# Optimization experiments

Measured on AMD Instinct MI355X. Metric: run time of the kernel, lower is better.

The kernel has to match this reference:

```python
import jax, jax.numpy as jnp
import numpy as np

B, L_Q, S_KV, H, E = 4, 1024, 1024, 8, 64
IN_CH = OUT_CH = 512
MODES = 64
INDEX_Q = np.arange(MODES)   # 'lowest' mode selection -> range(0, modes)
INDEX_KV = np.arange(MODES)
SCALE = 1.0 / np.sqrt(OUT_CH)
FACTOR = 5


def setup_inputs() -> dict:
    key = jax.random.key(0)
    ks = jax.random.split(key, 7)
    tf_queries = jax.random.normal(ks[0], (B, L_Q, H, E), jnp.float32)
    queries = jax.random.normal(ks[1], (B, L_Q, H, E), jnp.float32)
    keys = jax.random.normal(ks[2], (B, S_KV, H, E), jnp.float32)
    values = jax.random.normal(ks[3], (B, S_KV, H, E), jnp.float32)
    mask = jnp.ones((1,), jnp.int32)  # unused by the module
    weights_fuse = jax.random.uniform(ks[4], (H, L_Q, 2), jnp.float32)
    # torch.rand with cfloat dtype samples re/im independently from U[0,1)
    w1_re = SCALE * jax.random.uniform(ks[5], (H, IN_CH // 8, OUT_CH // 8, MODES), jnp.float32)
    w1_im = SCALE * jax.random.uniform(ks[6], (H, IN_CH // 8, OUT_CH // 8, MODES), jnp.float32)
    return dict(tf_queries=tf_queries, queries=queries, keys=keys, values=values,
                mask=mask, weights_fuse=weights_fuse, w1_re=w1_re, w1_im=w1_im)


def get_sig_scores(n, queries, keys, scale, corr):
    # queries/keys: [B, L, H, E] (keys already aligned to L_Q)
    B_, Lq, H_, E_ = queries.shape
    Lk = keys.shape[1]
    q = jnp.transpose(queries, (0, 2, 1, 3))  # [B,H,L,E]
    k = jnp.transpose(keys, (0, 2, 1, 3))
    if corr:
        qf = jnp.fft.rfft(jnp.transpose(queries, (0, 2, 3, 1)), axis=-1)
        kf = jnp.fft.rfft(jnp.transpose(keys, (0, 2, 3, 1)), axis=-1)
        autocorr = jnp.transpose(jnp.fft.irfft(qf * jnp.conj(kf), axis=-1), (0, 1, 3, 2))  # [B,H,L,E]
    else:
        autocorr = q
    amp = jnp.linalg.norm(autocorr, axis=-1)           # [B,H,L]
    _, top_idx = jax.lax.top_k(amp, n)                 # [B,H,n]
    q_sel = jnp.take_along_axis(q, top_idx[..., None], axis=2)  # [B,H,n,E]
    scores = jnp.einsum('bhnd,bhmd->bhnm', q_sel, k) * scale    # [B,H,n,Lk]
    full = jnp.full((B_, H_, Lq, Lk), -jnp.inf, scores.dtype)
    bi = jnp.arange(B_)[:, None, None]
    hi = jnp.arange(H_)[None, :, None]
    full = full.at[bi, hi, top_idx].set(scores)        # scatter selected query rows
    # softmax over the query axis for every key position (transpose(2,3))
    return jax.nn.softmax(jnp.swapaxes(full, 2, 3), axis=-1)  # [B,H,Lk,Lq]


def reference(tf_queries, queries, keys, values, mask, weights_fuse, w1_re, w1_im):
    B_, Lq, H_, E_ = queries.shape
    S_ = keys.shape[1]
    xq = jnp.transpose(queries, (0, 2, 3, 1))  # [B,H,E,L_Q]
    xk = jnp.transpose(keys, (0, 2, 3, 1))     # [B,H,E,S]
    if Lq > S_:
        pad = jnp.zeros((B_, Lq - S_, H_, E_), keys.dtype)
        keys2 = jnp.concatenate([keys, pad], axis=1)
        values2 = jnp.concatenate([values, pad], axis=1)
    else:
        keys2 = keys[:, :Lq]
        values2 = values[:, :Lq]
    n_top = min(int(FACTOR * np.ceil(np.log(Lq))), Lq)

    attn_t = get_sig_scores(n_top, queries, keys2, SCALE, corr=True)
    attn_tf = get_sig_scores(n_top, tf_queries, keys2, SCALE, corr=False)

    nw = jax.nn.softmax(weights_fuse, axis=-1)  # [H,L_Q,2]
    fused = nw[None, :, :, 0, None] * attn_t + nw[None, :, :, 1, None] * attn_tf
    # dropout(p=0.1) in eval mode -> identity

    xq_ft = jnp.fft.rfft(xq, axis=-1)[:, :, :, INDEX_Q]   # [B,H,E,M]
    xk_ft = jnp.fft.rfft(xk, axis=-1)[:, :, :, INDEX_KV]  # [B,H,E,M]
    xqk = jnp.tanh(jnp.einsum('bhex,bhey->bhxy', xq_ft, xk_ft))  # complex tanh
    xqkv = jnp.einsum('bhxy,bhey->bhex', xqk, xk_ft)
    w1 = w1_re + 1j * w1_im
    xqkvw = jnp.einsum('bhex,heox->bhox', xqkv, w1)        # [B,H,O,M]
    out_ft = jnp.zeros((B_, H_, E_, Lq // 2 + 1), xqkvw.dtype)
    out_ft = out_ft.at[:, :, :, INDEX_Q].set(xqkvw)
    out = jnp.fft.irfft(out_ft / IN_CH / OUT_CH, n=Lq, axis=-1)  # [B,H,E,L_Q]

    output = jnp.einsum('bhlm,bhmd->bhld', fused, jnp.transpose(values2, (0, 2, 1, 3)))
    output = jnp.transpose(output, (0, 1, 3, 2))  # [B,H,D,L_Q]
    return (output + out) * 0.5
```

## Files before the change

kernel.cpp:

```cpp
#include <hip/hip_runtime.h>
#include <math.h>

#define B_ 4
#define H_ 8
#define L_ 1024
#define E_ 64
#define NTOP 35
#define SCALE_ 0.04419417382415922f

__global__ __launch_bounds__(256) void k_stage(const float* __restrict__ q_g,
                                               const float* __restrict__ k_g,
                                               float* __restrict__ xtq,
                                               float* __restrict__ xtk) {
  __shared__ float tile[64][65];
  const int tc = blockIdx.x & 15;
  const int src = (blockIdx.x >> 4) & 1;
  const int bh = blockIdx.x >> 5;
  const int b = bh >> 3, h = bh & 7;
  const int t0 = tc * 64;
  const int tid = threadIdx.x;
  const float* in = src ? k_g : q_g;
  float* out = src ? xtk : xtq;

  for (int idx = tid; idx < 1024; idx += 256) {
    int t = idx >> 4, e4 = idx & 15;
    float4 v = reinterpret_cast<const float4*>(
        in + ((size_t)(b * L_ + t0 + t) * H_ + h) * E_)[e4];
    tile[t][e4 * 4 + 0] = v.x; tile[t][e4 * 4 + 1] = v.y;
    tile[t][e4 * 4 + 2] = v.z; tile[t][e4 * 4 + 3] = v.w;
  }
  __syncthreads();
  for (int idx = tid; idx < 1024; idx += 256) {
    int e = idx >> 4, t4 = idx & 15;
    float4 v = make_float4(tile[t4 * 4 + 0][e], tile[t4 * 4 + 1][e],
                           tile[t4 * 4 + 2][e], tile[t4 * 4 + 3][e]);
    reinterpret_cast<float4*>(out + ((size_t)(bh * 64 + e)) * 1024 + t0)[t4] = v;
  }
}

__global__ __launch_bounds__(512) void k_fft_c(const float* __restrict__ xtq,
                                               const float* __restrict__ xtk,
                                               float* __restrict__ amp2_part,
                                               float* __restrict__ qft,
                                               float* __restrict__ kft) {
  __shared__ __align__(16) float zre[4][1024], zim[4][1024];
  __shared__ float ctab[512], stab[512];
  const int eg = blockIdx.x & 15;
  const int bh = blockIdx.x >> 4;
  const int tid = threadIdx.x;
  const float TWO_PI_N = 6.283185307179586f / 1024.0f;

  if (tid < 512) {
    float s, c;
    sincosf(TWO_PI_N * (float)tid, &s, &c);
    ctab[tid] = c; stab[tid] = s;
  }
  for (int idx = tid; idx < 1024; idx += 512) {
    int ee = idx >> 8, t4 = idx & 255;
    size_t ro = ((size_t)(bh * 64 + eg * 4 + ee)) * 1024;
    float4 qv = reinterpret_cast<const float4*>(xtq + ro)[t4];
    float4 kv = reinterpret_cast<const float4*>(xtk + ro)[t4];
    *reinterpret_cast<float4*>(&zre[ee][t4 * 4]) = qv;
    *reinterpret_cast<float4*>(&zim[ee][t4 * 4]) = kv;
  }
  __syncthreads();

  for (int s = 0; s < 10; ++s) {
    const int half = 512 >> s;
#pragma unroll
    for (int it = 0; it < 4; ++it) {
      int idx = tid + it * 512;
      int ee = idx >> 9;
      int bf = idx & 511;
      int j = bf & (half - 1);
      int p0 = ((bf >> (9 - s)) << (10 - s)) + j;
      int p1 = p0 + half;
      float ur = zre[ee][p0], ui = zim[ee][p0];
      float vr = zre[ee][p1], vi = zim[ee][p1];
      float dr = ur - vr, di = ui - vi;
      zre[ee][p0] = ur + vr; zim[ee][p0] = ui + vi;
      int twi = j << s;
      float c = ctab[twi], sn = stab[twi];
      zre[ee][p1] = fmaf(dr, c, di * sn);
      zim[ee][p1] = fmaf(di, c, -dr * sn);
    }
    __syncthreads();
  }

  float pr[8], pi_[8];
#pragma unroll
  for (int it = 0; it < 8; ++it) {
    int idx = tid + it * 512;
    int ee = idx >> 10;
    int p = idx & 1023;
    int m = __brev((unsigned)p) >> 22;
    int mp = (1024 - m) & 1023;
    int pp = __brev((unsigned)mp) >> 22;
    float ar = zre[ee][p], ai = zim[ee][p];
    float br = zre[ee][pp], bi = zim[ee][pp];
    float qr = 0.5f * (ar + br), qi = 0.5f * (ai - bi);
    float kr = 0.5f * (ai + bi), ki = -0.5f * (ar - br);
    pr[it]  = fmaf(qr, kr, qi * ki);
    pi_[it] = fmaf(qi, kr, -qr * ki);
    if (m < 64) {
      size_t o = ((size_t)(bh * 64 + eg * 4 + ee) * 64 + m) * 2;
      qft[o] = qr; qft[o + 1] = qi;
      kft[o] = kr; kft[o + 1] = ki;
    }
  }
  __syncthreads();
#pragma unroll
  for (int it = 0; it < 8; ++it) {
    int idx = tid + it * 512;
    int ee = idx >> 10;
    int p = idx & 1023;
    zre[ee][p] = pr[it]; zim[ee][p] = pi_[it];
  }
  __syncthreads();

  for (int idx = tid; idx < 2048; idx += 512) {
    int u = idx >> 10;
    int p = idx & 1023;
    int e0 = 2 * u, e1 = 2 * u + 1;
    float s_r = zre[e0][p] - zim[e1][p];
    float s_i = zim[e0][p] + zre[e1][p];
    zre[e0][p] = s_r; zim[e0][p] = s_i;
  }
  __syncthreads();

  for (int s = 9; s >= 0; --s) {
    const int half = 512 >> s;
#pragma unroll
    for (int it = 0; it < 2; ++it) {
      int idx = tid + it * 512;
      int ee = (idx >> 9) * 2;
      int bf = idx & 511;
      int j = bf & (half - 1);
      int p0 = ((bf >> (9 - s)) << (10 - s)) + j;
      int p1 = p0 + half;
      int twi = j << s;
      float c = ctab[twi], sn = stab[twi];
      float ur = zre[ee][p0], ui = zim[ee][p0];
      float wr = zre[ee][p1], wi = zim[ee][p1];
      float vr = fmaf(wr, c, -wi * sn);
      float vi = fmaf(wi, c, wr * sn);
      zre[ee][p0] = ur + vr; zim[ee][p0] = ui + vi;
      zre[ee][p1] = ur - vr; zim[ee][p1] = ui - vi;
    }
    __syncthreads();
  }

  for (int t = tid; t < 1024; t += 512) {
    float r0 = zre[0][t], i0 = zim[0][t];
    float r2 = zre[2][t], i2 = zim[2][t];
    amp2_part[(size_t)(bh * 16 + eg) * 1024 + t] =
        fmaf(r0, r0, fmaf(i0, i0, fmaf(r2, r2, i2 * i2)));
  }
}

__global__ __launch_bounds__(256) void k_fft_s(const float* __restrict__ q_g,
                                               const float* __restrict__ k_g,
                                               float* __restrict__ amp2_part,
                                               float* __restrict__ qft,
                                               float* __restrict__ kft) {
  __shared__ float zre[4][1024], zim[4][1024];
  __shared__ float ctab[512], stab[512];
  const int eg = blockIdx.x & 15;
  const int bh = blockIdx.x >> 4;
  const int b = bh >> 3, h = bh & 7;
  const int tid = threadIdx.x;
  const float TWO_PI_N = 6.283185307179586f / 1024.0f;

  for (int j = tid; j < 512; j += 256) {
    float s, c;
    sincosf(TWO_PI_N * (float)j, &s, &c);
    ctab[j] = c; stab[j] = s;
  }
  for (int t = tid; t < 1024; t += 256) {
    size_t g4 = ((size_t)(b * L_ + t) * H_ + h) * 16 + eg;
    float4 qv = reinterpret_cast<const float4*>(q_g)[g4];
    float4 kv = reinterpret_cast<const float4*>(k_g)[g4];
    zre[0][t] = qv.x; zre[1][t] = qv.y; zre[2][t] = qv.z; zre[3][t] = qv.w;
    zim[0][t] = kv.x; zim[1][t] = kv.y; zim[2][t] = kv.z; zim[3][t] = kv.w;
  }
  __syncthreads();

  for (int s = 0; s < 10; ++s) {
    const int half = 512 >> s;
#pragma unroll
    for (int it = 0; it < 8; ++it) {
      int idx = tid + it * 256;
      int ee = idx >> 9;
      int bf = idx & 511;
      int j = bf & (half - 1);
      int p0 = ((bf >> (9 - s)) << (10 - s)) + j;
      int p1 = p0 + half;
      float ur = zre[ee][p0], ui = zim[ee][p0];
      float vr = zre[ee][p1], vi = zim[ee][p1];
      float dr = ur - vr, di = ui - vi;
      zre[ee][p0] = ur + vr; zim[ee][p0] = ui + vi;
      int twi = j << s;
      float c = ctab[twi], sn = stab[twi];
      zre[ee][p1] = fmaf(dr, c, di * sn);
      zim[ee][p1] = fmaf(di, c, -dr * sn);
    }
    __syncthreads();
  }

  float pr[16], pi_[16];
#pragma unroll
  for (int it = 0; it < 16; ++it) {
    int idx = tid + it * 256;
    int ee = idx >> 10;
    int p = idx & 1023;
    int m = __brev((unsigned)p) >> 22;
    int mp = (1024 - m) & 1023;
    int pp = __brev((unsigned)mp) >> 22;
    float ar = zre[ee][p], ai = zim[ee][p];
    float br = zre[ee][pp], bi = zim[ee][pp];
    float qr = 0.5f * (ar + br), qi = 0.5f * (ai - bi);
    float kr = 0.5f * (ai + bi), ki = -0.5f * (ar - br);
    pr[it]  = fmaf(qr, kr, qi * ki);
    pi_[it] = fmaf(qi, kr, -qr * ki);
    if (m < 64) {
      size_t o = ((size_t)(bh * 64 + eg * 4 + ee) * 64 + m) * 2;
      qft[o] = qr; qft[o + 1] = qi;
      kft[o] = kr; kft[o + 1] = ki;
    }
  }
  __syncthreads();
#pragma unroll
  for (int it = 0; it < 16; ++it) {
    int idx = tid + it * 256;
    int ee = idx >> 10;
    int p = idx & 1023;
    zre[ee][p] = pr[it]; zim[ee][p] = pi_[it];
  }
  __syncthreads();

  for (int idx = tid; idx < 2048; idx += 256) {
    int u = idx >> 10;
    int p = idx & 1023;
    int e0 = 2 * u, e1 = 2 * u + 1;
    float s_r = zre[e0][p] - zim[e1][p];
    float s_i = zim[e0][p] + zre[e1][p];
    zre[e0][p] = s_r; zim[e0][p] = s_i;
  }
  __syncthreads();

  for (int s = 9; s >= 0; --s) {
    const int half = 512 >> s;
#pragma unroll
    for (int it = 0; it < 4; ++it) {
      int idx = tid + it * 256;
      int ee = (idx >> 9) * 2;
      int bf = idx & 511;
      int j = bf & (half - 1);
      int p0 = ((bf >> (9 - s)) << (10 - s)) + j;
      int p1 = p0 + half;
      int twi = j << s;
      float c = ctab[twi], sn = stab[twi];
      float ur = zre[ee][p0], ui = zim[ee][p0];
      float wr = zre[ee][p1], wi = zim[ee][p1];
      float vr = fmaf(wr, c, -wi * sn);
      float vi = fmaf(wi, c, wr * sn);
      zre[ee][p0] = ur + vr; zim[ee][p0] = ui + vi;
      zre[ee][p1] = ur - vr; zim[ee][p1] = ui - vi;
    }
    __syncthreads();
  }

  for (int t = tid; t < 1024; t += 256) {
    float r0 = zre[0][t], i0 = zim[0][t];
    float r2 = zre[2][t], i2 = zim[2][t];
    amp2_part[(size_t)(bh * 16 + eg) * 1024 + t] =
        fmaf(r0, r0, fmaf(i0, i0, fmaf(r2, r2, i2 * i2)));
  }
}

__global__ __launch_bounds__(256) void k_topk(const float* __restrict__ amp2_part,
                                              const float* __restrict__ tfq,
                                              int* __restrict__ sel_ws) {
  __shared__ float amp[1024];
  __shared__ float wv_s[4];
  __shared__ int wi_s[4];
  __shared__ int winner_s;
  const int src = blockIdx.x & 1;
  const int bh = blockIdx.x >> 1;
  const int b = bh >> 3, h = bh & 7;
  const int tid = threadIdx.x;

  if (src == 0) {
    for (int t = tid; t < 1024; t += 256) {
      float s = 0.f;
#pragma unroll
      for (int c = 0; c < 16; ++c) s += amp2_part[(size_t)(bh * 16 + c) * 1024 + t];
      amp[t] = s;
    }
  } else {
    for (int l = tid; l < 1024; l += 256) {
      const float4* p4 = reinterpret_cast<const float4*>(
          &tfq[((size_t)(b * L_ + l) * H_ + h) * E_]);
      float s = 0.f;
#pragma unroll
      for (int e4 = 0; e4 < 16; ++e4) {
        float4 v = p4[e4];
        s += v.x * v.x + v.y * v.y + v.z * v.z + v.w * v.w;
      }
      amp[l] = s;
    }
  }
  __syncthreads();

  float bv = -1.f; int bi = tid;
#pragma unroll
  for (int kk = 0; kk < 4; ++kk) {
    int t = tid + kk * 256;
    float v = amp[t];
    if (v > bv) { bv = v; bi = t; }
  }
  const int lane = tid & 63, w = tid >> 6;

  for (int it = 0; it < NTOP; ++it) {
    float v = bv; int i = bi;
#pragma unroll
    for (int d = 1; d < 64; d <<= 1) {
      float ov = __shfl_xor(v, d);
      int oi = __shfl_xor(i, d);
      if (ov > v || (ov == v && oi < i)) { v = ov; i = oi; }
    }
    if (lane == 0) { wv_s[w] = v; wi_s[w] = i; }
    __syncthreads();
    if (tid == 0) {
      float fv = wv_s[0]; int fi = wi_s[0];
#pragma unroll
      for (int j = 1; j < 4; ++j) {
        if (wv_s[j] > fv || (wv_s[j] == fv && wi_s[j] < fi)) { fv = wv_s[j]; fi = wi_s[j]; }
      }
      winner_s = fi;
      sel_ws[(bh * 2 + src) * 64 + it] = fi;
    }
    __syncthreads();
    int fi = winner_s;
    if ((fi & 255) == tid) {
      amp[fi] = -1.f;
      bv = -1.f; bi = tid;
#pragma unroll
      for (int kk = 0; kk < 4; ++kk) {
        int t = tid + kk * 256;
        float vv = amp[t];
        if (vv > bv) { bv = vv; bi = t; }
      }
    }
  }
}

__global__ __launch_bounds__(256) void k_attn(const float* __restrict__ q_g,
                                              const float* __restrict__ tfq,
                                              const float* __restrict__ k_g,
                                              const float* __restrict__ v_g,
                                              const float* __restrict__ wfuse,
                                              const int* __restrict__ sel_ws,
                                              float* __restrict__ out) {
  __shared__ float4 qs4[2][NTOP][16];
  __shared__ float4 vs4[2][NTOP][16];
  const int ac = blockIdx.x & 15;
  const int bh = blockIdx.x >> 4;
  const int b = bh >> 3, h = bh & 7;
  const int a0 = ac * 64;
  const int tid = threadIdx.x;

  for (int idx = tid; idx < 2 * NTOP * 16; idx += 256) {
    int src = idx / (NTOP * 16);
    int rem = idx - src * (NTOP * 16);
    int i = rem >> 4, e4 = rem & 15;
    int row = sel_ws[(bh * 2 + src) * 64 + i];
    size_t rb = ((size_t)(b * L_ + row) * H_ + h) * E_;
    const float* qbase = src ? tfq : q_g;
    qs4[src][i][e4] = reinterpret_cast<const float4*>(qbase + rb)[e4];
    vs4[src][i][e4] = reinterpret_cast<const float4*>(v_g + rb)[e4];
  }
  __syncthreads();

  const int qd = tid & 3, r = tid >> 2;
  const int a = a0 + r;
  const int eb = qd * 16;

  size_t krb = ((size_t)(b * L_ + a) * H_ + h) * E_;
  const float4* k4p = reinterpret_cast<const float4*>(k_g + krb);
  float4 kq[4];
#pragma unroll
  for (int j4 = 0; j4 < 4; ++j4) kq[j4] = k4p[qd * 4 + j4];

  float ct[NTOP], ctf[NTOP];
#pragma unroll
  for (int i = 0; i < NTOP; ++i) { ct[i] = 0.f; ctf[i] = 0.f; }

#pragma unroll
  for (int j4 = 0; j4 < 4; ++j4) {
    float4 kv = kq[j4];
#pragma unroll
    for (int i = 0; i < NTOP; ++i) {
      float4 q4 = qs4[0][i][qd * 4 + j4];
      ct[i] = fmaf(q4.x, kv.x, ct[i]); ct[i] = fmaf(q4.y, kv.y, ct[i]);
      ct[i] = fmaf(q4.z, kv.z, ct[i]); ct[i] = fmaf(q4.w, kv.w, ct[i]);
      float4 p4 = qs4[1][i][qd * 4 + j4];
      ctf[i] = fmaf(p4.x, kv.x, ctf[i]); ctf[i] = fmaf(p4.y, kv.y, ctf[i]);
      ctf[i] = fmaf(p4.z, kv.z, ctf[i]); ctf[i] = fmaf(p4.w, kv.w, ctf[i]);
    }
  }
#pragma unroll
  for (int i = 0; i < NTOP; ++i) {
    ct[i] += __shfl_xor(ct[i], 1);  ct[i] += __shfl_xor(ct[i], 2);
    ctf[i] += __shfl_xor(ctf[i], 1); ctf[i] += __shfl_xor(ctf[i], 2);
  }

  float wf0 = wfuse[(h * L_ + a) * 2 + 0];
  float wf1 = wfuse[(h * L_ + a) * 2 + 1];
  float wm = fmaxf(wf0, wf1);
  float ew0 = expf(wf0 - wm), ew1 = expf(wf1 - wm);
  float nw0 = ew0 / (ew0 + ew1), nw1 = ew1 / (ew0 + ew1);

  {
    float m = -1e30f;
#pragma unroll
    for (int i = 0; i < NTOP; ++i) { ct[i] *= SCALE_; m = fmaxf(m, ct[i]); }
    float sum = 0.f;
#pragma unroll
    for (int i = 0; i < NTOP; ++i) { ct[i] = expf(ct[i] - m); sum += ct[i]; }
    float c = 0.5f * nw0 / sum;
#pragma unroll
    for (int i = 0; i < NTOP; ++i) ct[i] *= c;
  }
  {
    float m = -1e30f;
#pragma unroll
    for (int i = 0; i < NTOP; ++i) { ctf[i] *= SCALE_; m = fmaxf(m, ctf[i]); }
    float sum = 0.f;
#pragma unroll
    for (int i = 0; i < NTOP; ++i) { ctf[i] = expf(ctf[i] - m); sum += ctf[i]; }
    float c = 0.5f * nw1 / sum;
#pragma unroll
    for (int i = 0; i < NTOP; ++i) ctf[i] *= c;
  }
#pragma unroll
  for (int j4 = 0; j4 < 4; ++j4) {
    float ax = 0.f, ay = 0.f, az = 0.f, aw = 0.f;
#pragma unroll
    for (int i = 0; i < NTOP; ++i) {
      float4 v4 = vs4[0][i][qd * 4 + j4];
      ax = fmaf(ct[i], v4.x, ax); ay = fmaf(ct[i], v4.y, ay);
      az = fmaf(ct[i], v4.z, az); aw = fmaf(ct[i], v4.w, aw);
    }
#pragma unroll
    for (int i = 0; i < NTOP; ++i) {
      float4 v4 = vs4[1][i][qd * 4 + j4];
      ax = fmaf(ctf[i], v4.x, ax); ay = fmaf(ctf[i], v4.y, ay);
      az = fmaf(ctf[i], v4.z, az); aw = fmaf(ctf[i], v4.w, aw);
    }
    int d = eb + j4 * 4;
    out[((size_t)(bh * 64 + d + 0)) * 1024 + a] = ax;
    out[((size_t)(bh * 64 + d + 1)) * 1024 + a] = ay;
    out[((size_t)(bh * 64 + d + 2)) * 1024 + a] = az;
    out[((size_t)(bh * 64 + d + 3)) * 1024 + a] = aw;
  }
}

__global__ __launch_bounds__(256) void k_spec12(const float* __restrict__ qft,
                                                 const float* __restrict__ kft,
                                                 float* __restrict__ xre_g,
                                                 float* __restrict__ xim_g) {
  __shared__ float kre[64][65], kim[64][65];
  __shared__ float qre[64][8], qim[64][8];
  __shared__ float tre[8][64], tim[8][64];
  const int xc = blockIdx.x & 7;
  const int bh = blockIdx.x >> 3;
  const int tid = threadIdx.x;

  for (int idx = tid; idx < 4096; idx += 256) {
    int e = idx >> 6, y = idx & 63;
    size_t o = ((size_t)(bh * 64 + e) * 64 + y) * 2;
    kre[e][y] = kft[o]; kim[e][y] = kft[o + 1];
  }
  for (int idx = tid; idx < 512; idx += 256) {
    int e = idx >> 3, xl = idx & 7;
    size_t o = ((size_t)(bh * 64 + e) * 64 + xc * 8 + xl) * 2;
    qre[e][xl] = qft[o]; qim[e][xl] = qft[o + 1];
  }
  __syncthreads();

  const int y = tid & 63, xg = tid >> 6;
#pragma unroll
  for (int xi = 0; xi < 2; ++xi) {
    int xl = xg + xi * 4;
    float ar = 0.f, ai = 0.f;
    for (int e = 0; e < 64; ++e) {
      float a = qre[e][xl], b = qim[e][xl];
      float c = kre[e][y], d = kim[e][y];
      ar = fmaf(a, c, fmaf(-b, d, ar));
      ai = fmaf(a, d, fmaf(b, c, ai));
    }
    float trv, tiv;
    float x2 = 2.f * ar, y2 = 2.f * ai;
    if (fabsf(x2) > 30.f) {
      trv = copysignf(1.f, ar); tiv = 0.f;
    } else {
      float sh = sinhf(x2), ch = coshf(x2);
      float sn = sinf(y2), cs = cosf(y2);
      float dd = ch + cs;
      trv = sh / dd; tiv = sn / dd;
    }
    tre[xl][y] = trv; tim[xl][y] = tiv;
  }
  __syncthreads();

  const int e2 = tid & 63, xg2 = tid >> 6;
#pragma unroll
  for (int xi = 0; xi < 2; ++xi) {
    int xl = xg2 + xi * 4;
    float ar = 0.f, ai = 0.f;
    for (int yy = 0; yy < 64; ++yy) {
      float a = tre[xl][yy], b = tim[xl][yy];
      float c = kre[e2][yy], d = kim[e2][yy];
      ar = fmaf(a, c, fmaf(-b, d, ar));
      ai = fmaf(a, d, fmaf(b, c, ai));
    }
    xre_g[(size_t)bh * 4096 + (xc * 8 + xl) * 64 + e2] = ar;
    xim_g[(size_t)bh * 4096 + (xc * 8 + xl) * 64 + e2] = ai;
  }
}

__global__ __launch_bounds__(256) void k_w1(const float* __restrict__ xre_g,
                                            const float* __restrict__ xim_g,
                                            const float* __restrict__ w1re,
                                            const float* __restrict__ w1im,
                                            float* __restrict__ xw) {
  __shared__ float xre[64][65], xim[64][65];
  __shared__ float redr[4][512], redi[4][512];
  const int oc = blockIdx.x & 7;
  const int bh = blockIdx.x >> 3;
  const int h = bh & 7;
  const int tid = threadIdx.x;

  for (int idx = tid; idx < 4096; idx += 256) {
    int x = idx >> 6, e = idx & 63;
    xre[e][x] = xre_g[(size_t)bh * 4096 + idx];
    xim[e][x] = xim_g[(size_t)bh * 4096 + idx];
  }
  __syncthreads();

  const int x = tid & 63, g = tid >> 6;
  float accr[8], acci[8];
#pragma unroll
  for (int oo = 0; oo < 8; ++oo) { accr[oo] = 0.f; acci[oo] = 0.f; }

  for (int ee = 0; ee < 16; ++ee) {
    int e = g * 16 + ee;
    float a = xre[e][x], b = xim[e][x];
    size_t wbase = (((size_t)h * 64 + e) * 64 + oc * 8) * 64 + x;
#pragma unroll
    for (int oo = 0; oo < 8; ++oo) {
      float c = w1re[wbase + (size_t)oo * 64];
      float d = w1im[wbase + (size_t)oo * 64];
      accr[oo] = fmaf(a, c, fmaf(-b, d, accr[oo]));
      acci[oo] = fmaf(a, d, fmaf(b, c, acci[oo]));
    }
  }
#pragma unroll
  for (int oo = 0; oo < 8; ++oo) {
    redr[g][oo * 64 + x] = accr[oo];
    redi[g][oo * 64 + x] = acci[oo];
  }
  __syncthreads();

  const float INV = 1.0f / (512.0f * 512.0f);
  for (int idx = tid; idx < 512; idx += 256) {
    int oo = idx >> 6, x2 = idx & 63;
    float r = redr[0][idx] + redr[1][idx] + redr[2][idx] + redr[3][idx];
    float i = redi[0][idx] + redi[1][idx] + redi[2][idx] + redi[3][idx];
    size_t oidx = ((size_t)(bh * 64 + oc * 8 + oo) * 64 + x2) * 2;
    xw[oidx] = r * INV;
    xw[oidx + 1] = i * INV;
  }
}

__global__ __launch_bounds__(256) void k_final(const float* __restrict__ xw,
                                               float* __restrict__ out) {
  __shared__ float Xre[8][64], Xim[8][64];
  const int tc = blockIdx.x & 3;
  const int oc = (blockIdx.x >> 2) & 7;
  const int bh = blockIdx.x >> 5;
  const int o0 = oc * 8;
  const int tid = threadIdx.x;

  for (int idx = tid; idx < 512; idx += 256) {
    int o = idx >> 6, m = idx & 63;
    size_t s = ((size_t)(bh * 64 + o0 + o) * 64 + m) * 2;
    Xre[o][m] = 2.f * xw[s]; Xim[o][m] = 2.f * xw[s + 1];
  }
  __syncthreads();

  const int t = tc * 256 + tid;
  const float HALF_INVN = 0.5f / 1024.0f;
  const float TWO_PI = 6.283185307179586f;
  float th = TWO_PI * (float)t * (1.0f / 1024.0f);
  float s1, c1;
  __sincosf(th, &s1, &c1);
  float cm = c1, sm = s1;

  float acc[8];
#pragma unroll
  for (int o = 0; o < 8; ++o) acc[o] = 0.5f * Xre[o][0];

  for (int m = 1; m < 64; ++m) {
#pragma unroll
    for (int o = 0; o < 8; ++o) {
      acc[o] = fmaf(Xre[o][m], cm, acc[o]);
      acc[o] = fmaf(-Xim[o][m], sm, acc[o]);
    }
    float cn = fmaf(cm, c1, -sm * s1);
    float sn = fmaf(sm, c1, cm * s1);
    cm = cn; sm = sn;
  }
#pragma unroll
  for (int o = 0; o < 8; ++o) {
    size_t oi = ((size_t)(bh * 64 + o0 + o)) * 1024 + t;
    out[oi] = fmaf(acc[o], HALF_INVN, out[oi]);
  }
}

extern "C" void kernel_launch(void* const* d_in, const int* in_sizes, int n_in,
                              void* d_out, int out_size, void* d_ws, size_t ws_size,
                              hipStream_t stream) {
  const float* tfq   = (const float*)d_in[0];
  const float* q     = (const float*)d_in[1];
  const float* k     = (const float*)d_in[2];
  const float* v     = (const float*)d_in[3];
  const float* wfuse = (const float*)d_in[5];
  const float* w1re  = (const float*)d_in[6];
  const float* w1im  = (const float*)d_in[7];
  float* out = (float*)d_out;
  float* ws  = (float*)d_ws;

  const size_t STAGED_FLOATS = 5246976;
  if (ws_size >= STAGED_FLOATS * sizeof(float)) {
    float* xtq   = ws;
    float* xtk   = ws + 2097152;
    float* amp2  = ws + 4194304;
    float* qft   = ws + 4718592;
    float* kft   = ws + 4980736;
    int*   sel   = (int*)(ws + 5242880);
    float* xre_g = ws;
    float* xim_g = ws + 131072;
    float* xw    = ws + 262144;

    k_stage<<<1024, 256, 0, stream>>>(q, k, xtq, xtk);
    k_fft_c<<<512, 512, 0, stream>>>(xtq, xtk, amp2, qft, kft);
    k_topk<<<64, 256, 0, stream>>>(amp2, tfq, sel);
    k_attn<<<512, 256, 0, stream>>>(q, tfq, k, v, wfuse, sel, out);
    k_spec12<<<256, 256, 0, stream>>>(qft, kft, xre_g, xim_g);
    k_w1<<<256, 256, 0, stream>>>(xre_g, xim_g, w1re, w1im, xw);
    k_final<<<1024, 256, 0, stream>>>(xw, out);
  } else {
    float* amp2  = ws;
    float* xre_g = ws;
    float* xim_g = ws + 131072;
    float* xw    = ws + 262144;
    float* qft   = ws + 524288;
    float* kft   = ws + 786432;
    int*   sel   = (int*)(ws + 1048576);

    k_fft_s<<<512, 256, 0, stream>>>(q, k, amp2, qft, kft);
    k_topk<<<64, 256, 0, stream>>>(amp2, tfq, sel);
    k_attn<<<512, 256, 0, stream>>>(q, tfq, k, v, wfuse, sel, out);
    k_spec12<<<256, 256, 0, stream>>>(qft, kft, xre_g, xim_g);
    k_w1<<<256, 256, 0, stream>>>(xre_g, xim_g, w1re, w1im, xw);
    k_final<<<1024, 256, 0, stream>>>(xw, out);
  }
}
```

Before: 142.4 us.

## Split top-k into parallel reduction kernel and single-wavefront selection kernel

Replaces the 64-block k_topk with two kernels. k_red uses 160 blocks to sum the per-group spectral amplitude partials and compute the tf-query squared norms. k_sel then uses one 64-lane wavefront per (b,h,source) to run 35 rounds of register-resident argmax with shuffle reductions. This spreads the memory-bound amplitude work over more blocks and removes block-level synchronisation from the selection loop, at the cost of an extra launch and an intermediate buffer in workspace.

```diff
diff --git a/kernel.cpp b/kernel.cpp
--- a/kernel.cpp
+++ b/kernel.cpp
@@ -278,6 +278,74 @@
   }
 }
 
+__global__ __launch_bounds__(256) void k_red(const float* __restrict__ amp2_part,
+                                             const float* __restrict__ tfq,
+                                             float* __restrict__ ampsum) {
+  const int blk = blockIdx.x;
+  const int tid = threadIdx.x;
+  if (blk < 32) {
+    const int bh = blk;
+    for (int t = tid; t < 1024; t += 256) {
+      float s = 0.f;
+#pragma unroll
+      for (int c = 0; c < 16; ++c)
+        s += amp2_part[(size_t)(bh * 16 + c) * 1024 + t];
+      ampsum[(size_t)(bh * 2) * 1024 + t] = s;
+    }
+  } else {
+    const int idx = blk - 32;
+    const int bh = idx >> 2, qt = idx & 3;
+    const int b = bh >> 3, h = bh & 7;
+    const int l = qt * 256 + tid;
+    const float4* p4 = reinterpret_cast<const float4*>(
+        &tfq[((size_t)(b * L_ + l) * H_ + h) * E_]);
+    float s = 0.f;
+#pragma unroll
+    for (int e4 = 0; e4 < 16; ++e4) {
+      float4 v = p4[e4];
+      s += v.x * v.x + v.y * v.y + v.z * v.z + v.w * v.w;
+    }
+    ampsum[(size_t)(bh * 2 + 1) * 1024 + l] = s;
+  }
+}
+
+__global__ __launch_bounds__(64) void k_sel(const float* __restrict__ ampsum,
+                                            int* __restrict__ sel_ws) {
+  const int p = blockIdx.x;
+  const int lane = threadIdx.x;
+  float val[16];
+#pragma unroll
+  for (int j = 0; j < 16; ++j)
+    val[j] = ampsum[(size_t)p * 1024 + j * 64 + lane];
+
+  float bv = -1.f; int bi = lane;
+#pragma unroll
+  for (int j = 0; j < 16; ++j) {
+    if (val[j] > bv) { bv = val[j]; bi = j * 64 + lane; }
+  }
+
+  for (int it = 0; it < NTOP; ++it) {
+    float v = bv; int i = bi;
+#pragma unroll
+    for (int d = 1; d < 64; d <<= 1) {
+      float ov = __shfl_xor(v, d);
+      int oi = __shfl_xor(i, d);
+      if (ov > v || (ov == v && oi < i)) { v = ov; i = oi; }
+    }
+    if (lane == 0) sel_ws[p * 64 + it] = i;
+    if ((i & 63) == lane) {
+      int jr = i >> 6;
+#pragma unroll
+      for (int j = 0; j < 16; ++j) if (j == jr) val[j] = -1.f;
+      bv = -1.f; bi = lane;
+#pragma unroll
+      for (int j = 0; j < 16; ++j) {
+        if (val[j] > bv) { bv = val[j]; bi = j * 64 + lane; }
+      }
+    }
+  }
+}
+
 __global__ __launch_bounds__(256) void k_topk(const float* __restrict__ amp2_part,
                                               const float* __restrict__ tfq,
                                               int* __restrict__ sel_ws) {
@@ -642,21 +710,23 @@
   float* out = (float*)d_out;
   float* ws  = (float*)d_ws;
 
-  const size_t STAGED_FLOATS = 5246976;
+  const size_t STAGED_FLOATS = 5312512;
   if (ws_size >= STAGED_FLOATS * sizeof(float)) {
-    float* xtq   = ws;
-    float* xtk   = ws + 2097152;
-    float* amp2  = ws + 4194304;
-    float* qft   = ws + 4718592;
-    float* kft   = ws + 4980736;
-    int*   sel   = (int*)(ws + 5242880);
-    float* xre_g = ws;
-    float* xim_g = ws + 131072;
-    float* xw    = ws + 262144;
+    float* xtq    = ws;
+    float* xtk    = ws + 2097152;
+    float* amp2   = ws + 4194304;
+    float* qft    = ws + 4718592;
+    float* kft    = ws + 4980736;
+    int*   sel    = (int*)(ws + 5242880);
+    float* ampsum = ws + 5246976;
+    float* xre_g  = ws;
+    float* xim_g  = ws + 131072;
+    float* xw     = ws + 262144;
 
     k_stage<<<1024, 256, 0, stream>>>(q, k, xtq, xtk);
     k_fft_c<<<512, 512, 0, stream>>>(xtq, xtk, amp2, qft, kft);
-    k_topk<<<64, 256, 0, stream>>>(amp2, tfq, sel);
+    k_red<<<160, 256, 0, stream>>>(amp2, tfq, ampsum);
+    k_sel<<<64, 64, 0, stream>>>(ampsum, sel);
     k_attn<<<512, 256, 0, stream>>>(q, tfq, k, v, wfuse, sel, out);
     k_spec12<<<256, 256, 0, stream>>>(qft, kft, xre_g, xim_g);
     k_w1<<<256, 256, 0, stream>>>(xre_g, xim_g, w1re, w1im, xw);
```

New measurement: 134.0 us. 1.06x faster.
